# Optimization experiments

Measured on AMD Instinct MI355X. Metric: run time of the kernel, lower is better.

Reference implementation:

```python
import jax, jax.numpy as jnp
import numpy as np
import math

D_MODEL = 512
N_HEAD = 8
TAU = 0.5


def _leaky_integrate(x):
    # dx/dt = -x / tau; x + dx/dt  (with tau=0.5 this equals -x)
    return x + (-x / TAU)


def setup_inputs() -> dict:
    key = jax.random.key(0)
    ks = jax.random.split(key, 12)
    B, S, D = 4, 2048, D_MODEL
    s = 1.0 / math.sqrt(D)
    inp = {
        "query": jax.random.normal(ks[0], (B, S, D), jnp.float32),
        "key": jax.random.normal(ks[1], (B, S, D), jnp.float32),
        "value": jax.random.normal(ks[2], (B, S, D), jnp.float32),
        "Wq": jax.random.normal(ks[3], (D, D), jnp.float32) * s,
        "bq": jnp.zeros((D,), jnp.float32),
        "Wk": jax.random.normal(ks[4], (D, D), jnp.float32) * s,
        "bk": jnp.zeros((D,), jnp.float32),
        "Wv": jax.random.normal(ks[5], (D, D), jnp.float32) * s,
        "bv": jnp.zeros((D,), jnp.float32),
        "Wo": jax.random.normal(ks[6], (D, D), jnp.float32) * s,
        "bo": jnp.zeros((D,), jnp.float32),
    }
    return inp


def reference(query, key, value, Wq, bq, Wk, bk, Wv, bv, Wo, bo):
    B, S, D = query.shape
    H = N_HEAD
    dh = D // H
    # linear projections (torch Linear: x @ W^T + b)
    q = query @ Wq.T + bq
    k = key @ Wk.T + bk
    v = value @ Wv.T + bv
    # (B, S, D) -> (B, H, S, dh)
    q = q.reshape(B, S, H, dh).transpose(0, 2, 1, 3)
    k = k.reshape(B, S, H, dh).transpose(0, 2, 1, 3)
    v = v.reshape(B, S, H, dh).transpose(0, 2, 1, 3)
    # leaky integration on q, k
    q = _leaky_integrate(q)
    k = _leaky_integrate(k)
    # scores scaled by sqrt(d_model) (NOT head dim) per the source
    scores = jnp.einsum("bhsd,bhtd->bhst", q, k) / math.sqrt(D_MODEL)
    attn = jax.nn.softmax(scores, axis=-1)
    # conductance-based synapse: elementwise sigmoid AFTER softmax
    attn = jax.nn.sigmoid(attn)
    out = jnp.einsum("bhst,bhtd->bhsd", attn, v)
    out = out.transpose(0, 2, 1, 3).reshape(B, S, D)
    return out @ Wo.T + bo
```

## Files before the change

kernel.cpp:

```cpp
#include <hip/hip_runtime.h>
#include <stdint.h>
#include <math.h>

using u16    = unsigned short;
using short8 = __attribute__((ext_vector_type(8))) short;
using f32x4  = __attribute__((ext_vector_type(4))) float;
using f32x16 = __attribute__((ext_vector_type(16))) float;
using u32x4  = __attribute__((ext_vector_type(4))) uint32_t;

#define DEVI __device__ __forceinline__
#define FENCE asm volatile("" ::: "memory")
#define GPTR(p) ((const __attribute__((address_space(1))) uint32_t*)(p))
#define LPTR(p) ((__attribute__((address_space(3))) uint32_t*)(p))

static constexpr int S  = 2048;
static constexpr int D  = 512;
static constexpr int DH = 64;
static constexpr float C2 = 0.063763906f;

DEVI u16 f2bf(float f){
  uint32_t u = __float_as_uint(f);
  u = u + 0x7FFFu + ((u >> 16) & 1u);
  return (u16)(u >> 16);
}

DEVI uint32_t cvt_pk_bf16(float a, float b){
  uint32_t d;
  asm("v_cvt_pk_bf16_f32 %0, %1, %2" : "=v"(d) : "v"(a), "v"(b));
  return d;
}

__global__ void k_cvtw(const float* __restrict__ a, const float* __restrict__ b,
                       const float* __restrict__ c, const float* __restrict__ d,
                       u16* __restrict__ out){
  int i = blockIdx.x * blockDim.x + threadIdx.x;
  int sel = i >> 16;
  const float* src = sel == 0 ? a : sel == 1 ? b : sel == 2 ? c : d;
  float4 v = reinterpret_cast<const float4*>(src)[i & ((1<<16)-1)];
  uint2 o;
  o.x = (uint32_t)f2bf(v.x) | ((uint32_t)f2bf(v.y) << 16);
  o.y = (uint32_t)f2bf(v.z) | ((uint32_t)f2bf(v.w) << 16);
  reinterpret_cast<uint2*>(out)[i] = o;
}

__global__ __launch_bounds__(512)
void k_gemm_qkv(const float* __restrict__ Xq, const float* __restrict__ Xk,
                const float* __restrict__ Xv, const u16* __restrict__ Wall,
                const float* __restrict__ bq, const float* __restrict__ bk,
                const float* __restrict__ bv,
                u16* __restrict__ Qp, u16* __restrict__ Kp, u16* __restrict__ Vtp)
{
  __shared__ __align__(16) u16 As[2][128*64];
  __shared__ __align__(16) u16 Bs[2][128*64];
  const int tid = threadIdx.x;
  const int w = tid >> 6, l = tid & 63;
  const int wm = w & 3, wn = w >> 2;
  const int m0 = blockIdx.x * 128, n0 = blockIdx.y * 128;
  const int z = blockIdx.z;
  const int srow = l >> 3, sslot = l & 7;

  const float* X = z == 0 ? Xq : (z == 1 ? Xk : Xv);
  const u16*   W = Wall + (size_t)z * 512 * 512;
  const float* bias = z == 0 ? bq : (z == 1 ? bk : bv);
  const float oscale = z == 0 ? C2 : 1.0f;

  const int arow = tid >> 2;
  const int ac   = (tid & 3) * 16;

  f32x4 acc[2][4];
  #pragma unroll
  for (int i = 0; i < 2; i++)
    #pragma unroll
    for (int j = 0; j < 4; j++)
      #pragma unroll
      for (int r = 0; r < 4; r++) acc[i][j][r] = 0.f;

  float4 av[4];
  auto LOADA = [&](int kt){
    #pragma unroll
    for (int j = 0; j < 4; j++)
      av[j] = *reinterpret_cast<const float4*>(&X[(long)(m0 + arow)*D + kt + ac + j*4]);
  };
  auto WRITEA = [&](int buf){
    #pragma unroll
    for (int j2 = 0; j2 < 2; j2++){
      u32x4 p;
      p[0] = cvt_pk_bf16(av[2*j2].x,   av[2*j2].y);
      p[1] = cvt_pk_bf16(av[2*j2].z,   av[2*j2].w);
      p[2] = cvt_pk_bf16(av[2*j2+1].x, av[2*j2+1].y);
      p[3] = cvt_pk_bf16(av[2*j2+1].z, av[2*j2+1].w);
      int slot = ((ac >> 3) + j2) ^ (arow & 7);
      *reinterpret_cast<u32x4*>(&As[buf][arow*64 + slot*8]) = p;
    }
  };
  auto STAGEB = [&](int buf, int kt){
    #pragma unroll
    for (int i = 0; i < 2; i++){
      int r = w*16 + i*8 + srow;
      int scol = (sslot ^ (r & 7)) * 8;
      __builtin_amdgcn_global_load_lds(GPTR(W + (long)(n0 + r)*D + kt + scol),
                                       LPTR(&Bs[buf][(w*16 + i*8)*64]), 16, 0, 0);
    }
  };

  LOADA(0); STAGEB(0, 0);
  WRITEA(0);
  __syncthreads();

  for (int t = 0; t < 8; t++){
    int buf = t & 1;
    if (t < 7){ LOADA((t+1)*64); STAGEB(buf ^ 1, (t+1)*64); }
    #pragma unroll
    for (int ks = 0; ks < 2; ks++){
      short8 af[2];
      #pragma unroll
      for (int mf = 0; mf < 2; mf++){
        int row = wm*32 + mf*16 + (l & 15);
        int cw = (ks*4 + (l >> 4)) ^ (row & 7);
        af[mf] = *reinterpret_cast<const short8*>(&As[buf][(row*8 + cw)*8]);
      }
      #pragma unroll
      for (int nf = 0; nf < 4; nf++){
        int row = wn*64 + nf*16 + (l & 15);
        int cw = (ks*4 + (l >> 4)) ^ (row & 7);
        short8 bf = *reinterpret_cast<const short8*>(&Bs[buf][(row*8 + cw)*8]);
        #pragma unroll
        for (int mf = 0; mf < 2; mf++)
          acc[mf][nf] = __builtin_amdgcn_mfma_f32_16x16x32_bf16(af[mf], bf, acc[mf][nf], 0, 0, 0);
      }
    }
    if (t < 7) WRITEA(buf ^ 1);
    __syncthreads();
  }

  #pragma unroll
  for (int mf = 0; mf < 2; mf++){
    #pragma unroll
    for (int nf = 0; nf < 4; nf++){
      int n = n0 + wn*64 + nf*16 + (l & 15);
      float bi = bias[n];
      int h_ = n >> 6, d_ = n & 63;
      if (z == 2){
        int mb = m0 + wm*32 + mf*16 + (l >> 4)*4;
        int b_ = mb >> 11, s_ = mb & 2047;
        uint2 o;
        o.x = (uint32_t)f2bf(acc[mf][nf][0] + bi) | ((uint32_t)f2bf(acc[mf][nf][1] + bi) << 16);
        o.y = (uint32_t)f2bf(acc[mf][nf][2] + bi) | ((uint32_t)f2bf(acc[mf][nf][3] + bi) << 16);
        *reinterpret_cast<uint2*>(&Vtp[((long)((b_*8 + h_)*64 + d_))*2048 + s_]) = o;
      } else {
        u16* outp = z == 0 ? Qp : Kp;
        #pragma unroll
        for (int r = 0; r < 4; r++){
          int m = m0 + wm*32 + mf*16 + (l >> 4)*4 + r;
          int b_ = m >> 11, s_ = m & 2047;
          outp[((long)((b_*8 + h_)*2048 + s_))*64 + d_] = f2bf((acc[mf][nf][r] + bi)*oscale);
        }
      }
    }
  }
}

__global__ __launch_bounds__(512)
void k_gemm_ao(const u16* __restrict__ A, const u16* __restrict__ W,
               const float* __restrict__ bias2, float* __restrict__ outp)
{
  __shared__ __align__(16) u16 As[3][128*64];
  __shared__ __align__(16) u16 Bs[3][128*64];
  const int tid = threadIdx.x;
  const int w = tid >> 6, l = tid & 63;
  const int wm = w & 3, wn = w >> 2;
  const int m0 = blockIdx.x * 128, n0 = blockIdx.y * 128;
  const int srow = l >> 3, sslot = l & 7;

  f32x4 acc[2][4];
  #pragma unroll
  for (int i = 0; i < 2; i++)
    #pragma unroll
    for (int j = 0; j < 4; j++)
      #pragma unroll
      for (int r = 0; r < 4; r++) acc[i][j][r] = 0.f;

  auto STAGE = [&](int buf, int kt){
    #pragma unroll
    for (int i = 0; i < 2; i++){
      int r = w*16 + i*8 + srow;
      int scol = (sslot ^ (r & 7)) * 8;
      int m = m0 + r, k = kt + scol;
      long ga = ((long)(((m >> 11)*8 + (k >> 6))*2048 + (m & 2047)))*64 + (k & 63);
      __builtin_amdgcn_global_load_lds(GPTR(A + ga), LPTR(&As[buf][(w*16 + i*8)*64]), 16, 0, 0);
      long gb = (long)(n0 + r)*D + kt + scol;
      __builtin_amdgcn_global_load_lds(GPTR(W + gb), LPTR(&Bs[buf][(w*16 + i*8)*64]), 16, 0, 0);
    }
  };

  STAGE(0, 0); STAGE(1, 64);
  asm volatile("s_waitcnt vmcnt(4)" ::: "memory");
  __builtin_amdgcn_s_barrier();
  FENCE;

  #pragma unroll
  for (int t = 0; t < 8; t++){
    const int buf = t % 3;
    if (t + 2 < 8) STAGE((t + 2) % 3, (t + 2)*64);
    #pragma unroll
    for (int ks = 0; ks < 2; ks++){
      short8 af[2];
      #pragma unroll
      for (int mf = 0; mf < 2; mf++){
        int row = wm*32 + mf*16 + (l & 15);
        int cw = (ks*4 + (l >> 4)) ^ (row & 7);
        af[mf] = *reinterpret_cast<const short8*>(&As[buf][(row*8 + cw)*8]);
      }
      #pragma unroll
      for (int nf = 0; nf < 4; nf++){
        int row = wn*64 + nf*16 + (l & 15);
        int cw = (ks*4 + (l >> 4)) ^ (row & 7);
        short8 bf = *reinterpret_cast<const short8*>(&Bs[buf][(row*8 + cw)*8]);
        #pragma unroll
        for (int mf = 0; mf < 2; mf++)
          acc[mf][nf] = __builtin_amdgcn_mfma_f32_16x16x32_bf16(af[mf], bf, acc[mf][nf], 0, 0, 0);
      }
    }
    if (t < 7){
      if (t < 6) asm volatile("s_waitcnt vmcnt(4)" ::: "memory");
      else       asm volatile("s_waitcnt vmcnt(0)" ::: "memory");
      __builtin_amdgcn_s_barrier();
      FENCE;
    }
  }

  #pragma unroll
  for (int mf = 0; mf < 2; mf++)
    #pragma unroll
    for (int nf = 0; nf < 4; nf++){
      int n = n0 + wn*64 + nf*16 + (l & 15);
      float bi = bias2[(m0 >> 11)*512 + n];
      #pragma unroll
      for (int r = 0; r < 4; r++){
        int m = m0 + wm*32 + mf*16 + (l >> 4)*4 + r;
        outp[(long)m*D + n] = acc[mf][nf][r] + bi;
      }
    }
}

__global__ __launch_bounds__(256)
void k_sumv(const u16* __restrict__ Vt, float* __restrict__ SV){
  const int w = threadIdx.x >> 6, l = threadIdx.x & 63;
  const int row = blockIdx.x*4 + w;
  const u16* src = Vt + (long)row * S;
  float s = 0.f;
  #pragma unroll
  for (int j = 0; j < 4; j++){
    short8 v = *reinterpret_cast<const short8*>(&src[j*512 + l*8]);
    #pragma unroll
    for (int e = 0; e < 8; e++)
      s += __uint_as_float(((uint32_t)(u16)v[e]) << 16);
  }
  #pragma unroll
  for (int m = 1; m < 64; m <<= 1) s += __shfl_xor(s, m, 64);
  if (l == 0) SV[row] = s;
}

__global__ __launch_bounds__(256)
void k_bias2(const float* __restrict__ SV, const float* __restrict__ Wo,
             const float* __restrict__ bo, float* __restrict__ bias2){
  const int w = threadIdx.x >> 6, l = threadIdx.x & 63;
  const int idx = blockIdx.x*4 + w;
  const int b = idx >> 9, n = idx & 511;
  float dot = 0.f;
  #pragma unroll
  for (int j = 0; j < 2; j++){
    float4 wv = *reinterpret_cast<const float4*>(&Wo[(long)n*512 + l*8 + j*4]);
    float4 sv = *reinterpret_cast<const float4*>(&SV[b*512 + l*8 + j*4]);
    dot += wv.x*sv.x + wv.y*sv.y + wv.z*sv.z + wv.w*sv.w;
  }
  #pragma unroll
  for (int m = 1; m < 64; m <<= 1) dot += __shfl_xor(dot, m, 64);
  if (l == 0) bias2[idx] = bo[n] + 0.5f * dot;
}

__global__ __launch_bounds__(512, 4)
void k_flash(const u16* __restrict__ Qp, const u16* __restrict__ Kp,
             const u16* __restrict__ Vt, u16* __restrict__ AO)
{
  __shared__ __align__(16) u16 Ks[2][4][32*64];
  __shared__ __align__(16) u16 Vs[2][4][64*32];
  const int tid = threadIdx.x, w = tid >> 6, l = tid & 63;
  const int g = w >> 2, w4 = w & 3;
  const int bh = blockIdx.x & 31, qt = blockIdx.x >> 5;
  const u16* Qb = Qp + (long)bh * S * DH;
  const int hi = l >> 5, ln = l & 31;

  short8 qfr[4];
  #pragma unroll
  for (int c = 0; c < 4; c++){
    int row = qt*128 + w4*32 + ln;
    qfr[c] = *reinterpret_cast<const short8*>(&Qb[(long)row*DH + c*16 + hi*8]);
  }

  int koff[4], voff[4];
  #pragma unroll
  for (int c = 0; c < 4; c++)
    koff[c] = ln*64 + (((2*c + hi) ^ ((ln ^ (ln >> 3)) & 7))*8);
  #pragma unroll
  for (int ch = 0; ch < 2; ch++)
    #pragma unroll
    for (int nf = 0; nf < 2; nf++){
      int row = nf*32 + ln;
      voff[ch*2 + nf] = row*32 + (((2*ch + hi) ^ ((row ^ (row >> 2)) & 3))*8);
    }

  const u16* kptr = Kp + (long)bh*S*DH + g*2048;
  const u16* vptr = Vt + (long)bh*DH*S + g*32;
  const int rK = w4*8 + (l >> 3), sK = l & 7;
  const int rV = w4*16 + (l >> 2), sV = l & 3;
  const long ksrc = (long)rK*64 + ((sK ^ ((rK ^ (rK >> 3)) & 7))*8);
  const long vsrc = (long)rV*S  + ((sV ^ ((rV ^ (rV >> 2)) & 3))*8);

  auto STAGE = [&](int buf){
    __builtin_amdgcn_global_load_lds(GPTR(kptr + ksrc), LPTR(&Ks[g][buf][w4*512]), 16, 0, 0);
    __builtin_amdgcn_global_load_lds(GPTR(vptr + vsrc), LPTR(&Vs[g][buf][w4*512]), 16, 0, 0);
    kptr += 4096;
    vptr += 64;
  };

  f32x16 zero16;
  #pragma unroll
  for (int r = 0; r < 16; r++) zero16[r] = 0.f;
  f32x16 oacc[2];
  #pragma unroll
  for (int j = 0; j < 2; j++)
    #pragma unroll
    for (int r = 0; r < 16; r++) oacc[j][r] = 0.f;
  float lsum = 0.f;

  const u16* KB = &Ks[g][0][0];
  const u16* VB = &Vs[g][0][0];

  auto COMPUTE = [&](int buf){
    const u16* KT = KB + buf*2048;
    const u16* VT = VB + buf*2048;
    __builtin_amdgcn_s_setprio(1);
    short8 k0 = *reinterpret_cast<const short8*>(KT + koff[0]);
    f32x16 sacc = __builtin_amdgcn_mfma_f32_32x32x16_bf16(k0, qfr[0], zero16, 0, 0, 0);
    #pragma unroll
    for (int c = 1; c < 4; c++){
      short8 kfrag = *reinterpret_cast<const short8*>(KT + koff[c]);
      sacc = __builtin_amdgcn_mfma_f32_32x32x16_bf16(kfrag, qfr[c], sacc, 0, 0, 0);
    }
    __builtin_amdgcn_s_setprio(0);
    uint32_t pk[8];
    #pragma unroll
    for (int j = 0; j < 8; j++){
      float e0 = __builtin_amdgcn_exp2f(sacc[2*j]);
      float e1 = __builtin_amdgcn_exp2f(sacc[2*j+1]);
      lsum += e0 + e1;
      pk[j] = cvt_pk_bf16(e0, e1);
    }
    #pragma unroll
    for (int ch = 0; ch < 2; ch++){
      auto s1 = __builtin_amdgcn_permlane32_swap(pk[ch*4+0], pk[ch*4+2], false, false);
      auto s2 = __builtin_amdgcn_permlane32_swap(pk[ch*4+1], pk[ch*4+3], false, false);
      u32x4 av = { (uint32_t)s1[0], (uint32_t)s2[0], (uint32_t)s1[1], (uint32_t)s2[1] };
      short8 af = __builtin_bit_cast(short8, av);
      __builtin_amdgcn_s_setprio(1);
      #pragma unroll
      for (int nf = 0; nf < 2; nf++){
        short8 vfrag = *reinterpret_cast<const short8*>(VT + voff[ch*2 + nf]);
        oacc[nf] = __builtin_amdgcn_mfma_f32_32x32x16_bf16(af, vfrag, oacc[nf], 0, 0, 0);
      }
      __builtin_amdgcn_s_setprio(0);
    }
  };

  STAGE(0); STAGE(1); STAGE(2);
  asm volatile("s_waitcnt vmcnt(4)" ::: "memory");
  __builtin_amdgcn_s_barrier();
  FENCE;

  for (int tp = 0; tp < 7; tp++){
    #pragma unroll
    for (int tt = 0; tt < 4; tt++){
      STAGE((tt + 3) & 3);
      COMPUTE(tt);
      asm volatile("s_waitcnt vmcnt(4)" ::: "memory");
      __builtin_amdgcn_s_barrier();
      FENCE;
    }
  }
  STAGE(3);
  COMPUTE(0);
  asm volatile("s_waitcnt vmcnt(4)" ::: "memory");
  __builtin_amdgcn_s_barrier(); FENCE;
  COMPUTE(1);
  asm volatile("s_waitcnt vmcnt(2)" ::: "memory");
  __builtin_amdgcn_s_barrier(); FENCE;
  COMPUTE(2);
  asm volatile("s_waitcnt vmcnt(0)" ::: "memory");
  __builtin_amdgcn_s_barrier(); FENCE;
  COMPUTE(3);

  __syncthreads();

  lsum += __shfl_xor(lsum, 32, 64);
  float* OB = (float*)Ks;
  float* LB = (float*)Vs;
  if (g == 1){
    #pragma unroll
    for (int r = 0; r < 16; r++){
      int qrow = (r & 3) + 8*(r >> 2) + 4*hi;
      #pragma unroll
      for (int nf = 0; nf < 2; nf++)
        OB[w4*2048 + qrow*64 + nf*32 + ln] = oacc[nf][r];
    }
    if (hi == 0) LB[w4*32 + ln] = lsum;
  }
  __syncthreads();
  if (g == 0){
    float l2 = LB[w4*32 + ln];
    float linv = 0.25f / (lsum + l2);
    #pragma unroll
    for (int r = 0; r < 16; r++){
      int qrow = (r & 3) + 8*(r >> 2) + 4*hi;
      float sc = __shfl(linv, qrow, 64);
      int s_ = qt*128 + w4*32 + qrow;
      #pragma unroll
      for (int nf = 0; nf < 2; nf++){
        float o = oacc[nf][r] + OB[w4*2048 + qrow*64 + nf*32 + ln];
        AO[((long)bh*S + s_)*DH + nf*32 + ln] = f2bf(o * sc);
      }
    }
  }
}

extern "C" void kernel_launch(void* const* d_in, const int* in_sizes, int n_in,
                              void* d_out, int out_size, void* d_ws, size_t ws_size,
                              hipStream_t stream)
{
  const float* query = (const float*)d_in[0];
  const float* key_  = (const float*)d_in[1];
  const float* value = (const float*)d_in[2];
  const float* Wq = (const float*)d_in[3];
  const float* bq = (const float*)d_in[4];
  const float* Wk = (const float*)d_in[5];
  const float* bk = (const float*)d_in[6];
  const float* Wv = (const float*)d_in[7];
  const float* bv = (const float*)d_in[8];
  const float* Wo = (const float*)d_in[9];
  const float* bo = (const float*)d_in[10];

  char* ws = (char*)d_ws;
  const size_t XSZ = (size_t)8192 * 512 * 2;
  const size_t WSZ = (size_t)512 * 512 * 2;
  u16* AO  = (u16*)(ws);
  u16* wqb = (u16*)(ws + XSZ);
  u16* wob = (u16*)(ws + XSZ + 3*WSZ);
  u16* Qp  = (u16*)(ws + XSZ + 4*WSZ);
  u16* Kp  = (u16*)(ws + 2*XSZ + 4*WSZ);
  u16* Vtp = (u16*)(ws + 3*XSZ + 4*WSZ);
  float* SV    = (float*)(ws + 4*XSZ + 4*WSZ);
  float* bias2 = (float*)(ws + 4*XSZ + 4*WSZ + 8192);

  k_cvtw<<<(4<<16)/256, 256, 0, stream>>>(Wq, Wk, Wv, Wo, wqb);

  dim3 gq(64, 4, 3);
  k_gemm_qkv<<<gq, 512, 0, stream>>>(query, key_, value, wqb, bq, bk, bv, Qp, Kp, Vtp);

  k_sumv <<<512, 256, 0, stream>>>(Vtp, SV);
  k_bias2<<<512, 256, 0, stream>>>(SV, Wo, bo, bias2);

  k_flash<<<512, 512, 0, stream>>>(Qp, Kp, Vtp, AO);

  dim3 gg(64, 4);
  k_gemm_ao<<<gg, 512, 0, stream>>>(AO, wob, bias2, (float*)d_out);
}
```

Measured before the change: 95.55 us.

## Double query rows per flash block and deepen QKV GEMM A-prefetch

The flash kernel now has each wave handle two 32-row query slices, so every K/V tile staged in LDS serves twice as many queries. The grid halves to 256 blocks and launch bounds drop to 2 blocks per SM, which raises register pressure. The QKV GEMM double-buffers its A-operand register loads two tiles ahead and replaces __syncthreads with explicit waitcnt plus barrier to overlap global loads with MFMA. The risks are lower occupancy, fewer blocks than there are CUs to fill, and an epilogue that is now serialized per query half.

```diff
diff --git a/kernel.cpp b/kernel.cpp
--- a/kernel.cpp
+++ b/kernel.cpp
@@ -75,22 +75,22 @@
       #pragma unroll
       for (int r = 0; r < 4; r++) acc[i][j][r] = 0.f;
 
-  float4 av[4];
-  auto LOADA = [&](int kt){
+  float4 av[2][4];
+  auto LOADA = [&](int p, int kt){
     #pragma unroll
     for (int j = 0; j < 4; j++)
-      av[j] = *reinterpret_cast<const float4*>(&X[(long)(m0 + arow)*D + kt + ac + j*4]);
+      av[p][j] = *reinterpret_cast<const float4*>(&X[(long)(m0 + arow)*D + kt + ac + j*4]);
   };
-  auto WRITEA = [&](int buf){
+  auto WRITEA = [&](int buf, int p){
     #pragma unroll
     for (int j2 = 0; j2 < 2; j2++){
-      u32x4 p;
-      p[0] = cvt_pk_bf16(av[2*j2].x,   av[2*j2].y);
-      p[1] = cvt_pk_bf16(av[2*j2].z,   av[2*j2].w);
-      p[2] = cvt_pk_bf16(av[2*j2+1].x, av[2*j2+1].y);
-      p[3] = cvt_pk_bf16(av[2*j2+1].z, av[2*j2+1].w);
+      u32x4 pkv;
+      pkv[0] = cvt_pk_bf16(av[p][2*j2].x,   av[p][2*j2].y);
+      pkv[1] = cvt_pk_bf16(av[p][2*j2].z,   av[p][2*j2].w);
+      pkv[2] = cvt_pk_bf16(av[p][2*j2+1].x, av[p][2*j2+1].y);
+      pkv[3] = cvt_pk_bf16(av[p][2*j2+1].z, av[p][2*j2+1].w);
       int slot = ((ac >> 3) + j2) ^ (arow & 7);
-      *reinterpret_cast<u32x4*>(&As[buf][arow*64 + slot*8]) = p;
+      *reinterpret_cast<u32x4*>(&As[buf][arow*64 + slot*8]) = pkv;
     }
   };
   auto STAGEB = [&](int buf, int kt){
@@ -103,13 +103,19 @@
     }
   };
 
-  LOADA(0); STAGEB(0, 0);
-  WRITEA(0);
-  __syncthreads();
-
+  LOADA(0, 0);
+  STAGEB(0, 0);
+  WRITEA(0, 0);
+  LOADA(1, 64);
+  asm volatile("s_waitcnt vmcnt(4) lgkmcnt(0)" ::: "memory");
+  __builtin_amdgcn_s_barrier();
+  FENCE;
+
+  #pragma unroll
   for (int t = 0; t < 8; t++){
-    int buf = t & 1;
-    if (t < 7){ LOADA((t+1)*64); STAGEB(buf ^ 1, (t+1)*64); }
+    const int buf = t & 1;
+    if (t < 7) STAGEB(buf ^ 1, (t+1)*64);
+    if (t < 6) LOADA(t & 1, (t+2)*64);
     #pragma unroll
     for (int ks = 0; ks < 2; ks++){
       short8 af[2];
@@ -129,8 +135,10 @@
           acc[mf][nf] = __builtin_amdgcn_mfma_f32_16x16x32_bf16(af[mf], bf, acc[mf][nf], 0, 0, 0);
       }
     }
-    if (t < 7) WRITEA(buf ^ 1);
-    __syncthreads();
+    if (t < 7) WRITEA(buf ^ 1, (t+1) & 1);
+    if (t < 6)      asm volatile("s_waitcnt vmcnt(4) lgkmcnt(0)" ::: "memory");
+    else if (t == 6) asm volatile("s_waitcnt vmcnt(0) lgkmcnt(0)" ::: "memory");
+    if (t < 7){ __builtin_amdgcn_s_barrier(); FENCE; }
   }
 
   #pragma unroll
@@ -279,7 +287,7 @@
   if (l == 0) bias2[idx] = bo[n] + 0.5f * dot;
 }
 
-__global__ __launch_bounds__(512, 4)
+__global__ __launch_bounds__(512, 2)
 void k_flash(const u16* __restrict__ Qp, const u16* __restrict__ Kp,
              const u16* __restrict__ Vt, u16* __restrict__ AO)
 {
@@ -291,12 +299,14 @@
   const u16* Qb = Qp + (long)bh * S * DH;
   const int hi = l >> 5, ln = l & 31;
 
-  short8 qfr[4];
-  #pragma unroll
-  for (int c = 0; c < 4; c++){
-    int row = qt*128 + w4*32 + ln;
-    qfr[c] = *reinterpret_cast<const short8*>(&Qb[(long)row*DH + c*16 + hi*8]);
-  }
+  short8 qfr[2][4];
+  #pragma unroll
+  for (int qh = 0; qh < 2; qh++)
+    #pragma unroll
+    for (int c = 0; c < 4; c++){
+      int row = qt*256 + w4*64 + qh*32 + ln;
+      qfr[qh][c] = *reinterpret_cast<const short8*>(&Qb[(long)row*DH + c*16 + hi*8]);
+    }
 
   int koff[4], voff[4];
   #pragma unroll
@@ -327,12 +337,14 @@
   f32x16 zero16;
   #pragma unroll
   for (int r = 0; r < 16; r++) zero16[r] = 0.f;
-  f32x16 oacc[2];
-  #pragma unroll
-  for (int j = 0; j < 2; j++)
-    #pragma unroll
-    for (int r = 0; r < 16; r++) oacc[j][r] = 0.f;
-  float lsum = 0.f;
+  f32x16 oacc[2][2];
+  #pragma unroll
+  for (int qh = 0; qh < 2; qh++)
+    #pragma unroll
+    for (int j = 0; j < 2; j++)
+      #pragma unroll
+      for (int r = 0; r < 16; r++) oacc[qh][j][r] = 0.f;
+  float lsum[2] = {0.f, 0.f};
 
   const u16* KB = &Ks[g][0][0];
   const u16* VB = &Vs[g][0][0];
@@ -340,34 +352,47 @@
   auto COMPUTE = [&](int buf){
     const u16* KT = KB + buf*2048;
     const u16* VT = VB + buf*2048;
+    short8 kfr[4];
+    #pragma unroll
+    for (int c = 0; c < 4; c++)
+      kfr[c] = *reinterpret_cast<const short8*>(KT + koff[c]);
     __builtin_amdgcn_s_setprio(1);
-    short8 k0 = *reinterpret_cast<const short8*>(KT + koff[0]);
-    f32x16 sacc = __builtin_amdgcn_mfma_f32_32x32x16_bf16(k0, qfr[0], zero16, 0, 0, 0);
-    #pragma unroll
-    for (int c = 1; c < 4; c++){
-      short8 kfrag = *reinterpret_cast<const short8*>(KT + koff[c]);
-      sacc = __builtin_amdgcn_mfma_f32_32x32x16_bf16(kfrag, qfr[c], sacc, 0, 0, 0);
+    f32x16 sacc[2];
+    #pragma unroll
+    for (int qh = 0; qh < 2; qh++){
+      sacc[qh] = __builtin_amdgcn_mfma_f32_32x32x16_bf16(kfr[0], qfr[qh][0], zero16, 0, 0, 0);
+      #pragma unroll
+      for (int c = 1; c < 4; c++)
+        sacc[qh] = __builtin_amdgcn_mfma_f32_32x32x16_bf16(kfr[c], qfr[qh][c], sacc[qh], 0, 0, 0);
     }
     __builtin_amdgcn_s_setprio(0);
-    uint32_t pk[8];
-    #pragma unroll
-    for (int j = 0; j < 8; j++){
-      float e0 = __builtin_amdgcn_exp2f(sacc[2*j]);
-      float e1 = __builtin_amdgcn_exp2f(sacc[2*j+1]);
-      lsum += e0 + e1;
-      pk[j] = cvt_pk_bf16(e0, e1);
-    }
+    uint32_t pk[2][8];
+    #pragma unroll
+    for (int qh = 0; qh < 2; qh++)
+      #pragma unroll
+      for (int j = 0; j < 8; j++){
+        float e0 = __builtin_amdgcn_exp2f(sacc[qh][2*j]);
+        float e1 = __builtin_amdgcn_exp2f(sacc[qh][2*j+1]);
+        lsum[qh] += e0 + e1;
+        pk[qh][j] = cvt_pk_bf16(e0, e1);
+      }
     #pragma unroll
     for (int ch = 0; ch < 2; ch++){
-      auto s1 = __builtin_amdgcn_permlane32_swap(pk[ch*4+0], pk[ch*4+2], false, false);
-      auto s2 = __builtin_amdgcn_permlane32_swap(pk[ch*4+1], pk[ch*4+3], false, false);
-      u32x4 av = { (uint32_t)s1[0], (uint32_t)s2[0], (uint32_t)s1[1], (uint32_t)s2[1] };
-      short8 af = __builtin_bit_cast(short8, av);
+      short8 af[2];
+      #pragma unroll
+      for (int qh = 0; qh < 2; qh++){
+        auto s1 = __builtin_amdgcn_permlane32_swap(pk[qh][ch*4+0], pk[qh][ch*4+2], false, false);
+        auto s2 = __builtin_amdgcn_permlane32_swap(pk[qh][ch*4+1], pk[qh][ch*4+3], false, false);
+        u32x4 avv = { (uint32_t)s1[0], (uint32_t)s2[0], (uint32_t)s1[1], (uint32_t)s2[1] };
+        af[qh] = __builtin_bit_cast(short8, avv);
+      }
       __builtin_amdgcn_s_setprio(1);
       #pragma unroll
       for (int nf = 0; nf < 2; nf++){
         short8 vfrag = *reinterpret_cast<const short8*>(VT + voff[ch*2 + nf]);
-        oacc[nf] = __builtin_amdgcn_mfma_f32_32x32x16_bf16(af, vfrag, oacc[nf], 0, 0, 0);
+        #pragma unroll
+        for (int qh = 0; qh < 2; qh++)
+          oacc[qh][nf] = __builtin_amdgcn_mfma_f32_32x32x16_bf16(af[qh], vfrag, oacc[qh][nf], 0, 0, 0);
       }
       __builtin_amdgcn_s_setprio(0);
     }
@@ -402,34 +427,41 @@
 
   __syncthreads();
 
-  lsum += __shfl_xor(lsum, 32, 64);
+  lsum[0] += __shfl_xor(lsum[0], 32, 64);
+  lsum[1] += __shfl_xor(lsum[1], 32, 64);
+
   float* OB = (float*)Ks;
   float* LB = (float*)Vs;
-  if (g == 1){
-    #pragma unroll
-    for (int r = 0; r < 16; r++){
-      int qrow = (r & 3) + 8*(r >> 2) + 4*hi;
-      #pragma unroll
-      for (int nf = 0; nf < 2; nf++)
-        OB[w4*2048 + qrow*64 + nf*32 + ln] = oacc[nf][r];
-    }
-    if (hi == 0) LB[w4*32 + ln] = lsum;
-  }
-  __syncthreads();
-  if (g == 0){
-    float l2 = LB[w4*32 + ln];
-    float linv = 0.25f / (lsum + l2);
-    #pragma unroll
-    for (int r = 0; r < 16; r++){
-      int qrow = (r & 3) + 8*(r >> 2) + 4*hi;
-      float sc = __shfl(linv, qrow, 64);
-      int s_ = qt*128 + w4*32 + qrow;
-      #pragma unroll
-      for (int nf = 0; nf < 2; nf++){
-        float o = oacc[nf][r] + OB[w4*2048 + qrow*64 + nf*32 + ln];
-        AO[((long)bh*S + s_)*DH + nf*32 + ln] = f2bf(o * sc);
-      }
-    }
+
+  #pragma unroll
+  for (int qh = 0; qh < 2; qh++){
+    if (g == 1){
+      #pragma unroll
+      for (int r = 0; r < 16; r++){
+        int qrow = (r & 3) + 8*(r >> 2) + 4*hi;
+        #pragma unroll
+        for (int nf = 0; nf < 2; nf++)
+          OB[w4*2048 + qrow*64 + nf*32 + ln] = oacc[qh][nf][r];
+      }
+      if (hi == 0) LB[w4*32 + ln] = lsum[qh];
+    }
+    __syncthreads();
+    if (g == 0){
+      float lt = lsum[qh] + LB[w4*32 + ln];
+      float linv = 0.25f / lt;
+      #pragma unroll
+      for (int r = 0; r < 16; r++){
+        int qrow = (r & 3) + 8*(r >> 2) + 4*hi;
+        float sc = __shfl(linv, qrow, 64);
+        int s_ = qt*256 + w4*64 + qh*32 + qrow;
+        #pragma unroll
+        for (int nf = 0; nf < 2; nf++){
+          float o = oacc[qh][nf][r] + OB[w4*2048 + qrow*64 + nf*32 + ln];
+          AO[((long)bh*S + s_)*DH + nf*32 + ln] = f2bf(o * sc);
+        }
+      }
+    }
+    __syncthreads();
   }
 }
 
@@ -469,7 +501,7 @@
   k_sumv <<<512, 256, 0, stream>>>(Vtp, SV);
   k_bias2<<<512, 256, 0, stream>>>(SV, Wo, bo, bias2);
 
-  k_flash<<<512, 512, 0, stream>>>(Qp, Kp, Vtp, AO);
+  k_flash<<<256, 512, 0, stream>>>(Qp, Kp, Vtp, AO);
 
   dim3 gg(64, 4);
   k_gemm_ao<<<gg, 512, 0, stream>>>(AO, wob, bias2, (float*)d_out);
```

New measurement: 90.09 us. 1.06x faster.

## Software-pipeline QK^T one tile ahead of exp/PV and deepen projection A-prefetch

Applied to the files above, without the earlier changes.

The attention loop is split into QK, EXPPACK and PV stages. The QK MFMAs for tile t+1 are issued before exp and PV of tile t, using two alternating score accumulators, so matrix work can overlap the transcendental and permute work. The barrier and wait placement is moved to the top of each step. The projection GEMM now prefetches A two k-steps ahead with double-buffered registers and uses explicit waitcnt and barriers instead of __syncthreads. This raises register pressure, which may lower occupancy.

```diff
diff --git a/kernel.cpp b/kernel.cpp
--- a/kernel.cpp
+++ b/kernel.cpp
@@ -75,22 +75,22 @@
       #pragma unroll
       for (int r = 0; r < 4; r++) acc[i][j][r] = 0.f;
 
-  float4 av[4];
-  auto LOADA = [&](int kt){
+  float4 av[2][4];
+  auto LOADA = [&](int p, int kt){
     #pragma unroll
     for (int j = 0; j < 4; j++)
-      av[j] = *reinterpret_cast<const float4*>(&X[(long)(m0 + arow)*D + kt + ac + j*4]);
-  };
-  auto WRITEA = [&](int buf){
+      av[p][j] = *reinterpret_cast<const float4*>(&X[(long)(m0 + arow)*D + kt + ac + j*4]);
+  };
+  auto WRITEA = [&](int buf, int p){
     #pragma unroll
     for (int j2 = 0; j2 < 2; j2++){
-      u32x4 p;
-      p[0] = cvt_pk_bf16(av[2*j2].x,   av[2*j2].y);
-      p[1] = cvt_pk_bf16(av[2*j2].z,   av[2*j2].w);
-      p[2] = cvt_pk_bf16(av[2*j2+1].x, av[2*j2+1].y);
-      p[3] = cvt_pk_bf16(av[2*j2+1].z, av[2*j2+1].w);
+      u32x4 pkv;
+      pkv[0] = cvt_pk_bf16(av[p][2*j2].x,   av[p][2*j2].y);
+      pkv[1] = cvt_pk_bf16(av[p][2*j2].z,   av[p][2*j2].w);
+      pkv[2] = cvt_pk_bf16(av[p][2*j2+1].x, av[p][2*j2+1].y);
+      pkv[3] = cvt_pk_bf16(av[p][2*j2+1].z, av[p][2*j2+1].w);
       int slot = ((ac >> 3) + j2) ^ (arow & 7);
-      *reinterpret_cast<u32x4*>(&As[buf][arow*64 + slot*8]) = p;
+      *reinterpret_cast<u32x4*>(&As[buf][arow*64 + slot*8]) = pkv;
     }
   };
   auto STAGEB = [&](int buf, int kt){
@@ -103,13 +103,19 @@
     }
   };
 
-  LOADA(0); STAGEB(0, 0);
-  WRITEA(0);
-  __syncthreads();
-
+  LOADA(0, 0);
+  STAGEB(0, 0);
+  WRITEA(0, 0);
+  LOADA(1, 64);
+  asm volatile("s_waitcnt vmcnt(4) lgkmcnt(0)" ::: "memory");
+  __builtin_amdgcn_s_barrier();
+  FENCE;
+
+  #pragma unroll
   for (int t = 0; t < 8; t++){
-    int buf = t & 1;
-    if (t < 7){ LOADA((t+1)*64); STAGEB(buf ^ 1, (t+1)*64); }
+    const int buf = t & 1;
+    if (t < 7) STAGEB(buf ^ 1, (t+1)*64);
+    if (t < 6) LOADA(t & 1, (t+2)*64);
     #pragma unroll
     for (int ks = 0; ks < 2; ks++){
       short8 af[2];
@@ -129,8 +135,10 @@
           acc[mf][nf] = __builtin_amdgcn_mfma_f32_16x16x32_bf16(af[mf], bf, acc[mf][nf], 0, 0, 0);
       }
     }
-    if (t < 7) WRITEA(buf ^ 1);
-    __syncthreads();
+    if (t < 7) WRITEA(buf ^ 1, (t+1) & 1);
+    if (t < 6)      asm volatile("s_waitcnt vmcnt(4) lgkmcnt(0)" ::: "memory");
+    else if (t == 6) asm volatile("s_waitcnt vmcnt(0) lgkmcnt(0)" ::: "memory");
+    if (t < 7){ __builtin_amdgcn_s_barrier(); FENCE; }
   }
 
   #pragma unroll
@@ -310,23 +318,20 @@
       voff[ch*2 + nf] = row*32 + (((2*ch + hi) ^ ((row ^ (row >> 2)) & 3))*8);
     }
 
-  const u16* kptr = Kp + (long)bh*S*DH + g*2048;
-  const u16* vptr = Vt + (long)bh*DH*S + g*32;
   const int rK = w4*8 + (l >> 3), sK = l & 7;
   const int rV = w4*16 + (l >> 2), sV = l & 3;
-  const long ksrc = (long)rK*64 + ((sK ^ ((rK ^ (rK >> 3)) & 7))*8);
-  const long vsrc = (long)rV*S  + ((sV ^ ((rV ^ (rV >> 2)) & 3))*8);
+  const u16* kptr = Kp + (long)bh*S*DH + g*2048
+                  + (long)rK*64 + ((sK ^ ((rK ^ (rK >> 3)) & 7))*8);
+  const u16* vptr = Vt + (long)bh*DH*S + g*32
+                  + (long)rV*S  + ((sV ^ ((rV ^ (rV >> 2)) & 3))*8);
 
   auto STAGE = [&](int buf){
-    __builtin_amdgcn_global_load_lds(GPTR(kptr + ksrc), LPTR(&Ks[g][buf][w4*512]), 16, 0, 0);
-    __builtin_amdgcn_global_load_lds(GPTR(vptr + vsrc), LPTR(&Vs[g][buf][w4*512]), 16, 0, 0);
+    __builtin_amdgcn_global_load_lds(GPTR(kptr), LPTR(&Ks[g][buf][w4*512]), 16, 0, 0);
+    __builtin_amdgcn_global_load_lds(GPTR(vptr), LPTR(&Vs[g][buf][w4*512]), 16, 0, 0);
     kptr += 4096;
     vptr += 64;
   };
 
-  f32x16 zero16;
-  #pragma unroll
-  for (int r = 0; r < 16; r++) zero16[r] = 0.f;
   f32x16 oacc[2];
   #pragma unroll
   for (int j = 0; j < 2; j++)
@@ -337,68 +342,91 @@
   const u16* KB = &Ks[g][0][0];
   const u16* VB = &Vs[g][0][0];
 
-  auto COMPUTE = [&](int buf){
+  f32x16 saccA, saccB;
+  short8 paf[2];
+
+  auto QK = [&](int buf, f32x16& sacc){
     const u16* KT = KB + buf*2048;
-    const u16* VT = VB + buf*2048;
+    short8 kfr[4];
+    #pragma unroll
+    for (int c = 0; c < 4; c++)
+      kfr[c] = *reinterpret_cast<const short8*>(KT + koff[c]);
+    #pragma unroll
+    for (int r = 0; r < 16; r++) sacc[r] = 0.f;
     __builtin_amdgcn_s_setprio(1);
-    short8 k0 = *reinterpret_cast<const short8*>(KT + koff[0]);
-    f32x16 sacc = __builtin_amdgcn_mfma_f32_32x32x16_bf16(k0, qfr[0], zero16, 0, 0, 0);
-    #pragma unroll
-    for (int c = 1; c < 4; c++){
-      short8 kfrag = *reinterpret_cast<const short8*>(KT + koff[c]);
-      sacc = __builtin_amdgcn_mfma_f32_32x32x16_bf16(kfrag, qfr[c], sacc, 0, 0, 0);
-    }
+    #pragma unroll
+    for (int c = 0; c < 4; c++)
+      sacc = __builtin_amdgcn_mfma_f32_32x32x16_bf16(kfr[c], qfr[c], sacc, 0, 0, 0);
     __builtin_amdgcn_s_setprio(0);
+  };
+  auto EXPPACK = [&](f32x16& sacc){
     uint32_t pk[8];
+    float s0 = 0.f, s1 = 0.f;
     #pragma unroll
     for (int j = 0; j < 8; j++){
       float e0 = __builtin_amdgcn_exp2f(sacc[2*j]);
       float e1 = __builtin_amdgcn_exp2f(sacc[2*j+1]);
-      lsum += e0 + e1;
+      if (j & 1) s1 += e0 + e1; else s0 += e0 + e1;
       pk[j] = cvt_pk_bf16(e0, e1);
     }
+    lsum += s0 + s1;
     #pragma unroll
     for (int ch = 0; ch < 2; ch++){
-      auto s1 = __builtin_amdgcn_permlane32_swap(pk[ch*4+0], pk[ch*4+2], false, false);
-      auto s2 = __builtin_amdgcn_permlane32_swap(pk[ch*4+1], pk[ch*4+3], false, false);
-      u32x4 av = { (uint32_t)s1[0], (uint32_t)s2[0], (uint32_t)s1[1], (uint32_t)s2[1] };
-      short8 af = __builtin_bit_cast(short8, av);
-      __builtin_amdgcn_s_setprio(1);
+      auto p1 = __builtin_amdgcn_permlane32_swap(pk[ch*4+0], pk[ch*4+2], false, false);
+      auto p2 = __builtin_amdgcn_permlane32_swap(pk[ch*4+1], pk[ch*4+3], false, false);
+      u32x4 avv = { (uint32_t)p1[0], (uint32_t)p2[0], (uint32_t)p1[1], (uint32_t)p2[1] };
+      paf[ch] = __builtin_bit_cast(short8, avv);
+    }
+  };
+  auto PV = [&](int buf){
+    const u16* VT = VB + buf*2048;
+    __builtin_amdgcn_s_setprio(1);
+    #pragma unroll
+    for (int ch = 0; ch < 2; ch++)
       #pragma unroll
       for (int nf = 0; nf < 2; nf++){
         short8 vfrag = *reinterpret_cast<const short8*>(VT + voff[ch*2 + nf]);
-        oacc[nf] = __builtin_amdgcn_mfma_f32_32x32x16_bf16(af, vfrag, oacc[nf], 0, 0, 0);
-      }
-      __builtin_amdgcn_s_setprio(0);
-    }
+        oacc[nf] = __builtin_amdgcn_mfma_f32_32x32x16_bf16(paf[ch], vfrag, oacc[nf], 0, 0, 0);
+      }
+    __builtin_amdgcn_s_setprio(0);
   };
 
   STAGE(0); STAGE(1); STAGE(2);
   asm volatile("s_waitcnt vmcnt(4)" ::: "memory");
   __builtin_amdgcn_s_barrier();
   FENCE;
-
-  for (int tp = 0; tp < 7; tp++){
-    #pragma unroll
-    for (int tt = 0; tt < 4; tt++){
-      STAGE((tt + 3) & 3);
-      COMPUTE(tt);
-      asm volatile("s_waitcnt vmcnt(4)" ::: "memory");
+  QK(0, saccA);
+
+  #pragma unroll 1
+  for (int tp = 0; tp < 3; tp++){
+    #pragma unroll
+    for (int tt = 0; tt < 8; tt++){
+      asm volatile("s_waitcnt vmcnt(2)" ::: "memory");
       __builtin_amdgcn_s_barrier();
       FENCE;
-    }
-  }
-  STAGE(3);
-  COMPUTE(0);
-  asm volatile("s_waitcnt vmcnt(4)" ::: "memory");
-  __builtin_amdgcn_s_barrier(); FENCE;
-  COMPUTE(1);
+      STAGE((tt + 3) & 3);
+      if (tt & 1){ QK((tt + 1) & 3, saccA); EXPPACK(saccB); }
+      else       { QK((tt + 1) & 3, saccB); EXPPACK(saccA); }
+      PV(tt & 3);
+    }
+  }
+  #pragma unroll
+  for (int tt = 0; tt < 5; tt++){
+    asm volatile("s_waitcnt vmcnt(2)" ::: "memory");
+    __builtin_amdgcn_s_barrier();
+    FENCE;
+    STAGE((tt + 3) & 3);
+    if (tt & 1){ QK((tt + 1) & 3, saccA); EXPPACK(saccB); }
+    else       { QK((tt + 1) & 3, saccB); EXPPACK(saccA); }
+    PV(tt & 3);
+  }
   asm volatile("s_waitcnt vmcnt(2)" ::: "memory");
   __builtin_amdgcn_s_barrier(); FENCE;
-  COMPUTE(2);
+  QK(30 & 3, saccA); EXPPACK(saccB); PV(29 & 3);
   asm volatile("s_waitcnt vmcnt(0)" ::: "memory");
   __builtin_amdgcn_s_barrier(); FENCE;
-  COMPUTE(3);
+  QK(31 & 3, saccB); EXPPACK(saccA); PV(30 & 3);
+  EXPPACK(saccB); PV(31 & 3);
 
   __syncthreads();
 
```

New measurement: 117.7 us. 1.23x slower.
